# Performance work log

Measured on AMD Instinct MI355X. Metric: run time of the kernel, lower is better.

## Reference

```python
import jax, jax.numpy as jnp
import numpy as np


def bilinear_align_corners(p, H, W):
    # p: [B, C, h, w] -> [B, C, H, W], matches F.interpolate(mode='bilinear', align_corners=True)
    b, c, h, w = p.shape
    ys = jnp.linspace(0.0, h - 1.0, H)
    xs = jnp.linspace(0.0, w - 1.0, W)
    y0 = jnp.floor(ys).astype(jnp.int32)
    x0 = jnp.floor(xs).astype(jnp.int32)
    y1 = jnp.minimum(y0 + 1, h - 1)
    x1 = jnp.minimum(x0 + 1, w - 1)
    wy = (ys - y0.astype(p.dtype))[:, None]          # [H,1]
    wx = (xs - x0.astype(p.dtype))                   # [W]
    rows = p[:, :, y0, :] * (1 - wy) + p[:, :, y1, :] * wy   # [B,C,H,w]
    out = rows[:, :, :, x0] * (1 - wx) + rows[:, :, :, x1] * wx  # [B,C,H,W]
    return out


def conv1x1(x, W, b):
    return jnp.einsum('bchw,oc->bohw', x, W) + b[None, :, None, None]


def scan_axis(feat, A_bar, B_bar, axis):
    # selective recurrence h_i = A_i * stop_grad(h_{i-1}) + B_i * x_i along `axis`
    f = jnp.moveaxis(feat, axis, 0)
    A = jnp.moveaxis(A_bar, axis, 0)
    B = jnp.moveaxis(B_bar, axis, 0)

    def step(prev, inp):
        a_i, b_i, x_i = inp
        h = a_i * jax.lax.stop_gradient(prev) + b_i * x_i
        return h, h

    _, hs = jax.lax.scan(step, jnp.zeros_like(f[0]), (A, B, f))
    return jnp.moveaxis(hs, 0, axis)


def setup_inputs() -> dict:
    key = jax.random.key(0)
    ks = jax.random.split(key, 12)
    Bsz, Cin, H, W = 4, 64, 256, 256
    hid = 128
    s_in = 1.0 / np.sqrt(Cin)
    s_hid = 1.0 / np.sqrt(hid)
    return {
        'x': jax.random.normal(ks[0], (Bsz, Cin, H, W), jnp.float32),
        'prior': jax.random.normal(ks[1], (Bsz, 1, 64, 64), jnp.float32),
        'W_in': jax.random.uniform(ks[2], (hid, Cin), jnp.float32, -s_in, s_in),
        'b_in': jax.random.uniform(ks[3], (hid,), jnp.float32, -s_in, s_in),
        'W_out': jax.random.uniform(ks[4], (Cin, hid), jnp.float32, -s_hid, s_hid),
        'b_out': jax.random.uniform(ks[5], (Cin,), jnp.float32, -s_hid, s_hid),
        'W_delta': jax.random.uniform(ks[6], (hid, hid), jnp.float32, -s_hid, s_hid),
        'b_delta': jax.random.uniform(ks[7], (hid,), jnp.float32, -s_hid, s_hid),
        'W_B': jax.random.uniform(ks[8], (hid, hid), jnp.float32, -s_hid, s_hid),
        'b_B': jax.random.uniform(ks[9], (hid,), jnp.float32, -s_hid, s_hid),
        'A_param': jax.random.normal(ks[10], (hid,), jnp.float32),
        'lambda_delta': jnp.float32(0.1),
        'alpha': jnp.float32(0.1),
        'gamma': jnp.float32(0.1),
    }


def reference(x, prior, W_in, b_in, W_out, b_out, W_delta, b_delta, W_B, b_B,
              A_param, lambda_delta, alpha, gamma):
    Bsz, C, H, W = x.shape
    prior_up = jnp.clip(bilinear_align_corners(prior, H, W), -1.0, 1.0)
    x_proj = conv1x1(x, W_in, b_in)
    delta = jax.nn.softplus(conv1x1(x_proj, W_delta, b_delta) + lambda_delta * prior_up)
    B_k = conv1x1(x_proj, W_B, b_B) * (1.0 + alpha * prior_up)
    A = -jnp.exp(A_param)[None, :, None, None]
    A_bar = jnp.exp(delta * A)
    B_bar = delta * B_k
    # dim=0 in torch code scans along W (axis 3); dim=1 scans along H (axis 2)
    scanned = scan_axis(x_proj, A_bar, B_bar, 3) + scan_axis(x_proj, A_bar, B_bar, 2)
    out = conv1x1(scanned, W_out, b_out)
    return (x + gamma * out, prior_up)
```

## Files before the change

kernel.cpp:

```cpp
#include <hip/hip_runtime.h>
#include <hip/hip_bf16.h>

#define OUT1 16777216
#define BIG  33554432

typedef _Float16 half8 __attribute__((ext_vector_type(8)));
typedef float    floatx4 __attribute__((ext_vector_type(4)));

struct __align__(8) h4s { _Float16 x, y, z, w; };
struct __align__(16) au16 { h4s a, u; };

__global__ __launch_bounds__(256) void k_comb(const float* __restrict__ W_in, const float* __restrict__ b_in,
        const float* __restrict__ W_delta, const float* __restrict__ b_delta,
        const float* __restrict__ W_B, const float* __restrict__ b_B,
        const float* __restrict__ A_param, const float* __restrict__ W_out,
        _Float16* __restrict__ Wch, float* __restrict__ bcv, float* __restrict__ negA,
        _Float16* __restrict__ Wof, float* __restrict__ bct){
    int i = blockIdx.x*256 + threadIdx.x;
    if (i < 24576){
        int r = i >> 6, c = i & 63;
        float v;
        if (r < 128) v = W_in[i];
        else if (r < 256){
            int rr = r-128; float s = 0.f;
            for (int k=0;k<128;k++) s = fmaf(W_delta[(rr<<7)+k], W_in[(k<<6)+c], s);
            v = s;
        } else {
            int rr = r-256; float s = 0.f;
            for (int k=0;k<128;k++) s = fmaf(W_B[(rr<<7)+k], W_in[(k<<6)+c], s);
            v = s;
        }
        Wch[i] = (_Float16)v;
    } else if (i < 24960){
        int r = i - 24576; float v;
        if (r < 128) v = b_in[r];
        else if (r < 256){
            int rr=r-128; float s = b_delta[rr];
            for (int k=0;k<128;k++) s = fmaf(W_delta[(rr<<7)+k], b_in[k], s);
            v = s;
        } else {
            int rr=r-256; float s = b_B[rr];
            for (int k=0;k<128;k++) s = fmaf(W_B[(rr<<7)+k], b_in[k], s);
            v = s;
        }
        bcv[r] = v;
    } else if (i < 25088){
        negA[i-24960] = -expf(A_param[i-24960]);
    } else if (i < 33280){
        Wof[i-25088] = (_Float16)W_out[i-25088];
    } else if (i < 33792){
        int j = i - 33280;
        int c = j >> 2, comp = j & 3;
        float v;
        if (comp == 0) v = b_in[c];
        else if (comp == 1){
            float s = b_delta[c];
            for (int k=0;k<128;k++) s = fmaf(W_delta[(c<<7)+k], b_in[k], s);
            v = s;
        } else if (comp == 2){
            float s = b_B[c];
            for (int k=0;k<128;k++) s = fmaf(W_B[(c<<7)+k], b_in[k], s);
            v = s;
        } else {
            v = -expf(A_param[c]);
        }
        bct[j] = v;
    }
}

__global__ __launch_bounds__(512, 4) void k_proj_mfma(const float* __restrict__ x, const float* __restrict__ prior,
        const _Float16* __restrict__ Wch, const float* __restrict__ bct,
        const float* __restrict__ lam_p, const float* __restrict__ alp_p,
        float* __restrict__ pu, au16* __restrict__ AU){
    __shared__ _Float16 Ws[24576];

    const int t    = threadIdx.x;
    const int lane = t & 63;
    const int wave = t >> 6;
    const int col  = lane & 15;
    const int quad = lane >> 4;

    const int bl      = blockIdx.x;
    const int b       = bl >> 7;
    const int px_base = (bl & 127) << 9;

    {
        const float4* wsrc = (const float4*)Wch;
        #pragma unroll
        for (int i = 0; i < 6; i++){
            int c = t + (i << 9);
            int row = c >> 3, part = c & 7;
            float4 v = wsrc[c];
            int byteoff = ((row << 7) + (part << 4)) ^ ((row & 7) << 4);
            *(float4*)((char*)Ws + byteoff) = v;
        }
    }

    const float lamv = lam_p[0], alpv = alp_p[0];
    const float* xcol = x + ((size_t)b<<22) + col;

    float xf0[8], xf1[8];
    {
        const float* xp = xcol + px_base + (wave<<4);
        #pragma unroll
        for (int j = 0; j < 8; j++){
            xf0[j] = xp[(size_t)(quad*8 + j) << 16];
            xf1[j] = xp[(size_t)(quad*8 + j + 32) << 16];
        }
    }

    __syncthreads();

    const int qb = quad << 4;
    const char* wsb = (const char*)Ws;

    #pragma unroll 1
    for (int ch = 0; ch < 4; ch++){
        const int pxw = px_base + (ch << 7) + (wave << 4);

        half8 aX0, aX1;
        #pragma unroll
        for (int j = 0; j < 8; j++){
            aX0[j] = (_Float16)xf0[j];
            aX1[j] = (_Float16)xf1[j];
        }

        if (ch < 3){
            const float* xn = xcol + pxw + 128;
            #pragma unroll
            for (int j = 0; j < 8; j++){
                xf0[j] = xn[(size_t)(quad*8 + j) << 16];
                xf1[j] = xn[(size_t)(quad*8 + j + 32) << 16];
            }
        }

        const float scale = 63.0f/255.0f;
        int yy = pxw >> 8;
        float sy = yy*scale;
        int y0 = min((int)floorf(sy), 63);
        int y1 = min(y0+1, 63);
        float wy = sy - (float)y0;
        const float* pb0 = prior + (b<<12) + (y0<<6);
        const float* pb1 = prior + (b<<12) + (y1<<6);
        int xx0 = (pxw & 255) + (quad<<2);
        float lpu[4], apu[4];
        float4 puo;
        #pragma unroll
        for (int r = 0; r < 4; r++){
            float sx = (float)(xx0 + r)*scale;
            int x0 = min((int)floorf(sx), 63);
            int x1 = min(x0+1, 63);
            float wx = sx - (float)x0;
            float r0 = pb0[x0]*(1.f-wy) + pb1[x0]*wy;
            float r1 = pb0[x1]*(1.f-wy) + pb1[x1]*wy;
            float pv = fminf(fmaxf(r0*(1.f-wx) + r1*wx, -1.f), 1.f);
            ((float*)&puo)[r] = pv;
            lpu[r] = lamv * pv;
            apu[r] = fmaf(alpv, pv, 1.f);
        }
        *(float4*)(pu + (b<<16) + pxw + (quad<<2)) = puo;

        #pragma unroll 2
        for (int ct = 0; ct < 8; ct++){
            int rI = (ct << 4) + col;
            int xr = (rI & 7) << 4;
            half8 wI0 = *(const half8*)(wsb + ((( rI       << 7) +      qb) ^ xr));
            half8 wI1 = *(const half8*)(wsb + ((( rI       << 7) + 64 + qb) ^ xr));
            half8 wD0 = *(const half8*)(wsb + ((((rI + 128)<< 7) +      qb) ^ xr));
            half8 wD1 = *(const half8*)(wsb + ((((rI + 128)<< 7) + 64 + qb) ^ xr));
            half8 wB0 = *(const half8*)(wsb + ((((rI + 256)<< 7) +      qb) ^ xr));
            half8 wB1 = *(const half8*)(wsb + ((((rI + 256)<< 7) + 64 + qb) ^ xr));

            floatx4 aI = (floatx4){0.f,0.f,0.f,0.f};
            floatx4 aD = (floatx4){0.f,0.f,0.f,0.f};
            floatx4 aB = (floatx4){0.f,0.f,0.f,0.f};
            aI = __builtin_amdgcn_mfma_f32_16x16x32_f16(aX0, wI0, aI, 0, 0, 0);
            aD = __builtin_amdgcn_mfma_f32_16x16x32_f16(aX0, wD0, aD, 0, 0, 0);
            aB = __builtin_amdgcn_mfma_f32_16x16x32_f16(aX0, wB0, aB, 0, 0, 0);
            aI = __builtin_amdgcn_mfma_f32_16x16x32_f16(aX1, wI1, aI, 0, 0, 0);
            aD = __builtin_amdgcn_mfma_f32_16x16x32_f16(aX1, wD1, aD, 0, 0, 0);
            aB = __builtin_amdgcn_mfma_f32_16x16x32_f16(aX1, wB1, aB, 0, 0, 0);

            int c = (ct<<4) + col;
            float4 bv = *(const float4*)(bct + (c<<2));
            au16 ov;
            #pragma unroll
            for (int r = 0; r < 4; r++){
                float sI = aI[r] + bv.x;
                float sD = aD[r] + bv.y;
                float sB = aB[r] + bv.z;
                float dpre  = sD + lpu[r];
                float delta = fmaxf(dpre, 0.f) + __logf(1.f + __expf(-fabsf(dpre)));
                float ab    = __expf(bv.w * delta);
                float uu    = delta * sB * apu[r] * sI;
                (&ov.a.x)[r] = (_Float16)ab;
                (&ov.u.x)[r] = (_Float16)uu;
            }
            size_t u = (((size_t)((b<<7) + c)) << 14) + (pxw >> 2) + quad;
            AU[u] = ov;
        }
    }
}

__global__ __launch_bounds__(1024) void k_scan_wh(const au16* __restrict__ AU, _Float16* __restrict__ Sh){
    __shared__ _Float16 As2[16][256], Us2[16][256];
    __shared__ float    Wsc[16][256];
    __shared__ _Float16 Shs[16][256];

    const int t    = threadIdx.x;
    const int lane = t & 63;
    const int wave = t >> 6;
    const size_t plane = (size_t)blockIdx.x;
    const size_t bI = plane >> 7, cI = plane & 127;

    float Hcol = 0.f;

    const size_t ub = (plane << 14) + lane;

    au16 cur = AU[ub + ((size_t)wave << 6)];

    #pragma unroll 1
    for (int g = 0; g < 16; g++){
        au16 nxt = cur;
        if (g < 15) nxt = AU[ub + ((size_t)(((g + 1) << 4) + wave) << 6)];

        {
            float ax=(float)cur.a.x, ay=(float)cur.a.y, az=(float)cur.a.z, aw=(float)cur.a.w;
            float ux=(float)cur.u.x, uy=(float)cur.u.y, uz=(float)cur.u.z, uw=(float)cur.u.w;

            float A = ax, U = ux;
            U = fmaf(ay, U, uy); A *= ay;
            U = fmaf(az, U, uz); A *= az;
            U = fmaf(aw, U, uw); A *= aw;
            #pragma unroll
            for (int off=1; off<64; off<<=1){
                float Apv = __shfl_up(A, off, 64);
                float Upv = __shfl_up(U, off, 64);
                if (lane >= off){ U = fmaf(A, Upv, U); A *= Apv; }
            }
            float h = __shfl_up(U, 1, 64);
            if (lane == 0) h = 0.f;
            float4 o;
            h = fmaf(ax, h, ux); o.x = h;
            h = fmaf(ay, h, uy); o.y = h;
            h = fmaf(az, h, uz); o.z = h;
            h = fmaf(aw, h, uw); o.w = h;

            int c0 = lane << 2;
            *(h4s*)&As2[wave][c0] = cur.a;
            *(h4s*)&Us2[wave][c0] = cur.u;
            *(float4*)&Wsc[wave][c0] = o;
        }

        asm volatile("s_waitcnt lgkmcnt(0)" ::: "memory");
        __builtin_amdgcn_sched_barrier(0);
        __builtin_amdgcn_s_barrier();
        __builtin_amdgcn_sched_barrier(0);

        if (t < 256){
            #pragma unroll
            for (int v = 0; v < 16; v++){
                Hcol = fmaf((float)As2[v][t], Hcol, (float)Us2[v][t]);
                Shs[v][t] = (_Float16)(Hcol + Wsc[v][t]);
            }
        }

        asm volatile("s_waitcnt lgkmcnt(0)" ::: "memory");
        __builtin_amdgcn_sched_barrier(0);
        __builtin_amdgcn_s_barrier();
        __builtin_amdgcn_sched_barrier(0);

        {
            h4s sv = *(h4s*)&Shs[wave][lane << 2];
            size_t hh = (size_t)((g << 4) + wave);
            *(h4s*)(Sh + (bI<<23) + (hh<<15) + (cI<<8) + (lane<<2)) = sv;
        }

        cur = nxt;
    }
}

__global__ __launch_bounds__(256, 4) void k_out_mfma(const float* __restrict__ x, const _Float16* __restrict__ Sh,
        const _Float16* __restrict__ Wof, const float* __restrict__ bout, const float* __restrict__ gam_p,
        float* __restrict__ out){
    const int t    = threadIdx.x;
    const int lane = t & 63;
    const int wave = t >> 6;
    const int col  = lane & 15;
    const int quad = lane >> 4;
    const int b    = blockIdx.x >> 8;
    const int hh   = blockIdx.x & 255;
    const int p0   = hh << 8;
    const int wn0  = wave << 6;

    const _Float16* shb = Sh + ((size_t)b<<23) + ((size_t)hh<<15);

    floatx4 acc[4][4];
    #pragma unroll
    for (int mt = 0; mt < 4; mt++)
        #pragma unroll
        for (int nt = 0; nt < 4; nt++)
            acc[mt][nt] = (floatx4){0.f,0.f,0.f,0.f};

    #pragma unroll
    for (int kc = 0; kc < 4; kc++){
        half8 af[4];
        #pragma unroll
        for (int mt = 0; mt < 4; mt++)
            #pragma unroll
            for (int j = 0; j < 8; j++)
                af[mt][j] = shb[((kc*32 + quad*8 + j)<<8) + wn0 + mt*16 + col];
        half8 bf[4];
        #pragma unroll
        for (int nt = 0; nt < 4; nt++)
            bf[nt] = *(const half8*)(Wof + (nt*16 + col)*128 + kc*32 + quad*8);
        #pragma unroll
        for (int mt = 0; mt < 4; mt++)
            #pragma unroll
            for (int nt = 0; nt < 4; nt++)
                acc[mt][nt] = __builtin_amdgcn_mfma_f32_16x16x32_f16(af[mt], bf[nt], acc[mt][nt], 0, 0, 0);
    }

    const float gv = gam_p[0];
    #pragma unroll
    for (int nt = 0; nt < 4; nt++){
        int o = nt*16 + col;
        float bo = bout[o];
        #pragma unroll
        for (int mt = 0; mt < 4; mt++){
            size_t idx = (((size_t)(b*64 + o))<<16) + p0 + wn0 + mt*16 + (quad<<2);
            float4 xv = *(const float4*)(x + idx);
            float4 ov;
            ov.x = fmaf(gv, acc[mt][nt][0] + bo, xv.x);
            ov.y = fmaf(gv, acc[mt][nt][1] + bo, xv.y);
            ov.z = fmaf(gv, acc[mt][nt][2] + bo, xv.z);
            ov.w = fmaf(gv, acc[mt][nt][3] + bo, xv.w);
            *(float4*)(out + idx) = ov;
        }
    }
}

extern "C" void kernel_launch(void* const* d_in, const int* in_sizes, int n_in,
                              void* d_out, int out_size, void* d_ws, size_t ws_size,
                              hipStream_t stream){
    const float* x       = (const float*)d_in[0];
    const float* prior   = (const float*)d_in[1];
    const float* W_in    = (const float*)d_in[2];
    const float* b_in    = (const float*)d_in[3];
    const float* W_out   = (const float*)d_in[4];
    const float* b_out   = (const float*)d_in[5];
    const float* W_delta = (const float*)d_in[6];
    const float* b_delta = (const float*)d_in[7];
    const float* W_B     = (const float*)d_in[8];
    const float* b_B     = (const float*)d_in[9];
    const float* A_param = (const float*)d_in[10];
    const float* lam     = (const float*)d_in[11];
    const float* alp     = (const float*)d_in[12];
    const float* gam     = (const float*)d_in[13];

    float* out = (float*)d_out;
    float* pu  = out + OUT1;

    float* ws        = (float*)d_ws;
    _Float16* Wch    = (_Float16*)ws;
    float* bcv       = ws + 12288;
    float* negA      = ws + 12672;
    _Float16* Wof    = (_Float16*)(ws + 12800);
    float* bct       = ws + 16896;
    au16* AU         = (au16*)(ws + 32768);
    _Float16* Sh     = (_Float16*)(AU + BIG/4);

    hipLaunchKernelGGL(k_comb,   dim3(132),   dim3(256), 0, stream, W_in, b_in, W_delta, b_delta,
                       W_B, b_B, A_param, W_out, Wch, bcv, negA, Wof, bct);
    hipLaunchKernelGGL(k_proj_mfma, dim3(512), dim3(512), 0, stream,
                       x, prior, Wch, bct, lam, alp, pu, AU);
    hipLaunchKernelGGL(k_scan_wh, dim3(512), dim3(1024), 0, stream, AU, Sh);
    hipLaunchKernelGGL(k_out_mfma, dim3(1024), dim3(256), 0, stream, x, Sh, Wof, b_out, gam, out);
}
```

Baseline: 270.3 us.

## Fuse projection, scan and output kernels into one cooperative persistent kernel

Merges the projection, 2D scan and output projection kernels into one cooperative kernel of 256 blocks × 1024 threads. Grid-wide syncs separate the phases, and the phases share one LDS union. Each block now handles two of the old projection blocks, two scan planes and four output tiles, which removes two kernel launches and their gaps. It also drops the unused bias and negA precompute from the weight-combine kernel. The costs are lower occupancy than the separate launches, grid.sync overhead, and a 1024-thread block for the MFMA phases, which may raise register pressure under the launch bound.

Result: slower. 620.6 us (+129.6%).

```diff
diff --git a/kernel.cpp b/kernel.cpp
--- a/kernel.cpp
+++ b/kernel.cpp
@@ -1,8 +1,11 @@
 #include <hip/hip_runtime.h>
 #include <hip/hip_bf16.h>
+#include <hip/hip_cooperative_groups.h>
 
 #define OUT1 16777216
 #define BIG  33554432
+
+namespace cg = cooperative_groups;
 
 typedef _Float16 half8 __attribute__((ext_vector_type(8)));
 typedef float    floatx4 __attribute__((ext_vector_type(4)));
@@ -14,8 +17,7 @@
         const float* __restrict__ W_delta, const float* __restrict__ b_delta,
         const float* __restrict__ W_B, const float* __restrict__ b_B,
         const float* __restrict__ A_param, const float* __restrict__ W_out,
-        _Float16* __restrict__ Wch, float* __restrict__ bcv, float* __restrict__ negA,
-        _Float16* __restrict__ Wof, float* __restrict__ bct){
+        _Float16* __restrict__ Wch, _Float16* __restrict__ Wof, float* __restrict__ bct){
     int i = blockIdx.x*256 + threadIdx.x;
     if (i < 24576){
         int r = i >> 6, c = i & 63;
@@ -31,25 +33,10 @@
             v = s;
         }
         Wch[i] = (_Float16)v;
-    } else if (i < 24960){
-        int r = i - 24576; float v;
-        if (r < 128) v = b_in[r];
-        else if (r < 256){
-            int rr=r-128; float s = b_delta[rr];
-            for (int k=0;k<128;k++) s = fmaf(W_delta[(rr<<7)+k], b_in[k], s);
-            v = s;
-        } else {
-            int rr=r-256; float s = b_B[rr];
-            for (int k=0;k<128;k++) s = fmaf(W_B[(rr<<7)+k], b_in[k], s);
-            v = s;
-        }
-        bcv[r] = v;
-    } else if (i < 25088){
-        negA[i-24960] = -expf(A_param[i-24960]);
+    } else if (i < 32768){
+        Wof[i-24576] = (_Float16)W_out[i-24576];
     } else if (i < 33280){
-        Wof[i-25088] = (_Float16)W_out[i-25088];
-    } else if (i < 33792){
-        int j = i - 33280;
+        int j = i - 32768;
         int c = j >> 2, comp = j & 3;
         float v;
         if (comp == 0) v = b_in[c];
@@ -68,274 +55,280 @@
     }
 }
 
-__global__ __launch_bounds__(512, 4) void k_proj_mfma(const float* __restrict__ x, const float* __restrict__ prior,
+union MegaLds {
+    _Float16 Ws[24576];
+    struct {
+        _Float16 As2[16][256], Us2[16][256];
+        float    Wsc[16][256];
+        _Float16 Shs[16][256];
+    } s;
+};
+
+__global__ __launch_bounds__(1024, 4) void k_mega(const float* __restrict__ x, const float* __restrict__ prior,
         const _Float16* __restrict__ Wch, const float* __restrict__ bct,
         const float* __restrict__ lam_p, const float* __restrict__ alp_p,
-        float* __restrict__ pu, au16* __restrict__ AU){
-    __shared__ _Float16 Ws[24576];
+        float* __restrict__ pu, au16* __restrict__ AU, _Float16* __restrict__ Sh,
+        const _Float16* __restrict__ Wof, const float* __restrict__ bout,
+        const float* __restrict__ gam_p, float* __restrict__ out){
+    __shared__ MegaLds L;
+    cg::grid_group grid = cg::this_grid();
 
     const int t    = threadIdx.x;
     const int lane = t & 63;
-    const int wave = t >> 6;
+    const int w16  = t >> 6;
     const int col  = lane & 15;
     const int quad = lane >> 4;
-
-    const int bl      = blockIdx.x;
-    const int b       = bl >> 7;
-    const int px_base = (bl & 127) << 9;
 
     {
         const float4* wsrc = (const float4*)Wch;
         #pragma unroll
-        for (int i = 0; i < 6; i++){
-            int c = t + (i << 9);
+        for (int i = 0; i < 3; i++){
+            int c = t + (i << 10);
             int row = c >> 3, part = c & 7;
             float4 v = wsrc[c];
             int byteoff = ((row << 7) + (part << 4)) ^ ((row & 7) << 4);
-            *(float4*)((char*)Ws + byteoff) = v;
+            *(float4*)((char*)L.Ws + byteoff) = v;
+        }
+
+        const float lamv = lam_p[0], alpv = alp_p[0];
+        const int qb = quad << 4;
+        const char* wsb = (const char*)L.Ws;
+        bool staged_sync = false;
+
+        #pragma unroll 1
+        for (int sp = 0; sp < 2; sp++){
+            const int bl      = blockIdx.x*2 + sp;
+            const int b       = bl >> 7;
+            const int px_base = (bl & 127) << 9;
+            const float* xcol = x + ((size_t)b<<22) + col;
+
+            float xf0[8], xf1[8];
+            {
+                const float* xp = xcol + px_base + (w16<<4);
+                #pragma unroll
+                for (int j = 0; j < 8; j++){
+                    xf0[j] = xp[(size_t)(quad*8 + j) << 16];
+                    xf1[j] = xp[(size_t)(quad*8 + j + 32) << 16];
+                }
+            }
+            if (!staged_sync){ __syncthreads(); staged_sync = true; }
+
+            #pragma unroll 1
+            for (int ch = 0; ch < 2; ch++){
+                const int pxw = px_base + (ch << 8) + (w16 << 4);
+
+                half8 aX0, aX1;
+                #pragma unroll
+                for (int j = 0; j < 8; j++){
+                    aX0[j] = (_Float16)xf0[j];
+                    aX1[j] = (_Float16)xf1[j];
+                }
+                if (ch < 1){
+                    const float* xn = xcol + pxw + 256;
+                    #pragma unroll
+                    for (int j = 0; j < 8; j++){
+                        xf0[j] = xn[(size_t)(quad*8 + j) << 16];
+                        xf1[j] = xn[(size_t)(quad*8 + j + 32) << 16];
+                    }
+                }
+
+                const float scale = 63.0f/255.0f;
+                int yy = pxw >> 8;
+                float sy = yy*scale;
+                int y0 = min((int)floorf(sy), 63);
+                int y1 = min(y0+1, 63);
+                float wy = sy - (float)y0;
+                const float* pb0 = prior + (b<<12) + (y0<<6);
+                const float* pb1 = prior + (b<<12) + (y1<<6);
+                int xx0 = (pxw & 255) + (quad<<2);
+                float lpu[4], apu[4];
+                float4 puo;
+                #pragma unroll
+                for (int r = 0; r < 4; r++){
+                    float sx = (float)(xx0 + r)*scale;
+                    int x0 = min((int)floorf(sx), 63);
+                    int x1 = min(x0+1, 63);
+                    float wx = sx - (float)x0;
+                    float r0 = pb0[x0]*(1.f-wy) + pb1[x0]*wy;
+                    float r1 = pb0[x1]*(1.f-wy) + pb1[x1]*wy;
+                    float pv = fminf(fmaxf(r0*(1.f-wx) + r1*wx, -1.f), 1.f);
+                    ((float*)&puo)[r] = pv;
+                    lpu[r] = lamv * pv;
+                    apu[r] = fmaf(alpv, pv, 1.f);
+                }
+                *(float4*)(pu + (b<<16) + pxw + (quad<<2)) = puo;
+
+                #pragma unroll 2
+                for (int ct = 0; ct < 8; ct++){
+                    int rI = (ct << 4) + col;
+                    int xr = (rI & 7) << 4;
+                    half8 wI0 = *(const half8*)(wsb + ((( rI       << 7) +      qb) ^ xr));
+                    half8 wI1 = *(const half8*)(wsb + ((( rI       << 7) + 64 + qb) ^ xr));
+                    half8 wD0 = *(const half8*)(wsb + ((((rI + 128)<< 7) +      qb) ^ xr));
+                    half8 wD1 = *(const half8*)(wsb + ((((rI + 128)<< 7) + 64 + qb) ^ xr));
+                    half8 wB0 = *(const half8*)(wsb + ((((rI + 256)<< 7) +      qb) ^ xr));
+                    half8 wB1 = *(const half8*)(wsb + ((((rI + 256)<< 7) + 64 + qb) ^ xr));
+
+                    floatx4 aI = (floatx4){0.f,0.f,0.f,0.f};
+                    floatx4 aD = (floatx4){0.f,0.f,0.f,0.f};
+                    floatx4 aB = (floatx4){0.f,0.f,0.f,0.f};
+                    aI = __builtin_amdgcn_mfma_f32_16x16x32_f16(aX0, wI0, aI, 0, 0, 0);
+                    aD = __builtin_amdgcn_mfma_f32_16x16x32_f16(aX0, wD0, aD, 0, 0, 0);
+                    aB = __builtin_amdgcn_mfma_f32_16x16x32_f16(aX0, wB0, aB, 0, 0, 0);
+                    aI = __builtin_amdgcn_mfma_f32_16x16x32_f16(aX1, wI1, aI, 0, 0, 0);
+                    aD = __builtin_amdgcn_mfma_f32_16x16x32_f16(aX1, wD1, aD, 0, 0, 0);
+                    aB = __builtin_amdgcn_mfma_f32_16x16x32_f16(aX1, wB1, aB, 0, 0, 0);
+
+                    int c = (ct<<4) + col;
+                    float4 bv = *(const float4*)(bct + (c<<2));
+                    au16 ov;
+                    #pragma unroll
+                    for (int r = 0; r < 4; r++){
+                        float sI = aI[r] + bv.x;
+                        float sD = aD[r] + bv.y;
+                        float sB = aB[r] + bv.z;
+                        float dpre  = sD + lpu[r];
+                        float delta = fmaxf(dpre, 0.f) + __logf(1.f + __expf(-fabsf(dpre)));
+                        float ab    = __expf(bv.w * delta);
+                        float uu    = delta * sB * apu[r] * sI;
+                        (&ov.a.x)[r] = (_Float16)ab;
+                        (&ov.u.x)[r] = (_Float16)uu;
+                    }
+                    size_t u = (((size_t)((b<<7) + c)) << 14) + (pxw >> 2) + quad;
+                    AU[u] = ov;
+                }
+            }
         }
     }
 
-    const float lamv = lam_p[0], alpv = alp_p[0];
-    const float* xcol = x + ((size_t)b<<22) + col;
-
-    float xf0[8], xf1[8];
+    __threadfence();
+    grid.sync();
+
+    #pragma unroll 1
+    for (int pp = 0; pp < 2; pp++){
+        const size_t plane = (size_t)(blockIdx.x*2 + pp);
+        const size_t bI = plane >> 7, cI = plane & 127;
+        float Hcol = 0.f;
+        const size_t ub = (plane << 14) + lane;
+
+        au16 cur = AU[ub + ((size_t)w16 << 6)];
+
+        #pragma unroll 1
+        for (int g = 0; g < 16; g++){
+            au16 nxt = cur;
+            if (g < 15) nxt = AU[ub + ((size_t)(((g + 1) << 4) + w16) << 6)];
+
+            {
+                float ax=(float)cur.a.x, ay=(float)cur.a.y, az=(float)cur.a.z, aw=(float)cur.a.w;
+                float ux=(float)cur.u.x, uy=(float)cur.u.y, uz=(float)cur.u.z, uw=(float)cur.u.w;
+
+                float A = ax, U = ux;
+                U = fmaf(ay, U, uy); A *= ay;
+                U = fmaf(az, U, uz); A *= az;
+                U = fmaf(aw, U, uw); A *= aw;
+                #pragma unroll
+                for (int off=1; off<64; off<<=1){
+                    float Apv = __shfl_up(A, off, 64);
+                    float Upv = __shfl_up(U, off, 64);
+                    if (lane >= off){ U = fmaf(A, Upv, U); A *= Apv; }
+                }
+                float h = __shfl_up(U, 1, 64);
+                if (lane == 0) h = 0.f;
+                float4 o;
+                h = fmaf(ax, h, ux); o.x = h;
+                h = fmaf(ay, h, uy); o.y = h;
+                h = fmaf(az, h, uz); o.z = h;
+                h = fmaf(aw, h, uw); o.w = h;
+
+                int c0 = lane << 2;
+                *(h4s*)&L.s.As2[w16][c0] = cur.a;
+                *(h4s*)&L.s.Us2[w16][c0] = cur.u;
+                *(float4*)&L.s.Wsc[w16][c0] = o;
+            }
+
+            asm volatile("s_waitcnt lgkmcnt(0)" ::: "memory");
+            __builtin_amdgcn_sched_barrier(0);
+            __builtin_amdgcn_s_barrier();
+            __builtin_amdgcn_sched_barrier(0);
+
+            if (t < 256){
+                #pragma unroll
+                for (int v = 0; v < 16; v++){
+                    Hcol = fmaf((float)L.s.As2[v][t], Hcol, (float)L.s.Us2[v][t]);
+                    L.s.Shs[v][t] = (_Float16)(Hcol + L.s.Wsc[v][t]);
+                }
+            }
+
+            asm volatile("s_waitcnt lgkmcnt(0)" ::: "memory");
+            __builtin_amdgcn_sched_barrier(0);
+            __builtin_amdgcn_s_barrier();
+            __builtin_amdgcn_sched_barrier(0);
+
+            {
+                h4s sv = *(h4s*)&L.s.Shs[w16][lane << 2];
+                size_t hh = (size_t)((g << 4) + w16);
+                *(h4s*)(Sh + (bI<<23) + (hh<<15) + (cI<<8) + (lane<<2)) = sv;
+            }
+
+            cur = nxt;
+        }
+    }
+
+    __threadfence();
+    grid.sync();
+
     {
-        const float* xp = xcol + px_base + (wave<<4);
-        #pragma unroll
-        for (int j = 0; j < 8; j++){
-            xf0[j] = xp[(size_t)(quad*8 + j) << 16];
-            xf1[j] = xp[(size_t)(quad*8 + j + 32) << 16];
-        }
-    }
-
-    __syncthreads();
-
-    const int qb = quad << 4;
-    const char* wsb = (const char*)Ws;
-
-    #pragma unroll 1
-    for (int ch = 0; ch < 4; ch++){
-        const int pxw = px_base + (ch << 7) + (wave << 4);
-
-        half8 aX0, aX1;
-        #pragma unroll
-        for (int j = 0; j < 8; j++){
-            aX0[j] = (_Float16)xf0[j];
-            aX1[j] = (_Float16)xf1[j];
-        }
-
-        if (ch < 3){
-            const float* xn = xcol + pxw + 128;
-            #pragma unroll
-            for (int j = 0; j < 8; j++){
-                xf0[j] = xn[(size_t)(quad*8 + j) << 16];
-                xf1[j] = xn[(size_t)(quad*8 + j + 32) << 16];
-            }
-        }
-
-        const float scale = 63.0f/255.0f;
-        int yy = pxw >> 8;
-        float sy = yy*scale;
-        int y0 = min((int)floorf(sy), 63);
-        int y1 = min(y0+1, 63);
-        float wy = sy - (float)y0;
-        const float* pb0 = prior + (b<<12) + (y0<<6);
-        const float* pb1 = prior + (b<<12) + (y1<<6);
-        int xx0 = (pxw & 255) + (quad<<2);
-        float lpu[4], apu[4];
-        float4 puo;
-        #pragma unroll
-        for (int r = 0; r < 4; r++){
-            float sx = (float)(xx0 + r)*scale;
-            int x0 = min((int)floorf(sx), 63);
-            int x1 = min(x0+1, 63);
-            float wx = sx - (float)x0;
-            float r0 = pb0[x0]*(1.f-wy) + pb1[x0]*wy;
-            float r1 = pb0[x1]*(1.f-wy) + pb1[x1]*wy;
-            float pv = fminf(fmaxf(r0*(1.f-wx) + r1*wx, -1.f), 1.f);
-            ((float*)&puo)[r] = pv;
-            lpu[r] = lamv * pv;
-            apu[r] = fmaf(alpv, pv, 1.f);
-        }
-        *(float4*)(pu + (b<<16) + pxw + (quad<<2)) = puo;
-
-        #pragma unroll 2
-        for (int ct = 0; ct < 8; ct++){
-            int rI = (ct << 4) + col;
-            int xr = (rI & 7) << 4;
-            half8 wI0 = *(const half8*)(wsb + ((( rI       << 7) +      qb) ^ xr));
-            half8 wI1 = *(const half8*)(wsb + ((( rI       << 7) + 64 + qb) ^ xr));
-            half8 wD0 = *(const half8*)(wsb + ((((rI + 128)<< 7) +      qb) ^ xr));
-            half8 wD1 = *(const half8*)(wsb + ((((rI + 128)<< 7) + 64 + qb) ^ xr));
-            half8 wB0 = *(const half8*)(wsb + ((((rI + 256)<< 7) +      qb) ^ xr));
-            half8 wB1 = *(const half8*)(wsb + ((((rI + 256)<< 7) + 64 + qb) ^ xr));
-
-            floatx4 aI = (floatx4){0.f,0.f,0.f,0.f};
-            floatx4 aD = (floatx4){0.f,0.f,0.f,0.f};
-            floatx4 aB = (floatx4){0.f,0.f,0.f,0.f};
-            aI = __builtin_amdgcn_mfma_f32_16x16x32_f16(aX0, wI0, aI, 0, 0, 0);
-            aD = __builtin_amdgcn_mfma_f32_16x16x32_f16(aX0, wD0, aD, 0, 0, 0);
-            aB = __builtin_amdgcn_mfma_f32_16x16x32_f16(aX0, wB0, aB, 0, 0, 0);
-            aI = __builtin_amdgcn_mfma_f32_16x16x32_f16(aX1, wI1, aI, 0, 0, 0);
-            aD = __builtin_amdgcn_mfma_f32_16x16x32_f16(aX1, wD1, aD, 0, 0, 0);
-            aB = __builtin_amdgcn_mfma_f32_16x16x32_f16(aX1, wB1, aB, 0, 0, 0);
-
-            int c = (ct<<4) + col;
-            float4 bv = *(const float4*)(bct + (c<<2));
-            au16 ov;
-            #pragma unroll
-            for (int r = 0; r < 4; r++){
-                float sI = aI[r] + bv.x;
-                float sD = aD[r] + bv.y;
-                float sB = aB[r] + bv.z;
-                float dpre  = sD + lpu[r];
-                float delta = fmaxf(dpre, 0.f) + __logf(1.f + __expf(-fabsf(dpre)));
-                float ab    = __expf(bv.w * delta);
-                float uu    = delta * sB * apu[r] * sI;
-                (&ov.a.x)[r] = (_Float16)ab;
-                (&ov.u.x)[r] = (_Float16)uu;
-            }
-            size_t u = (((size_t)((b<<7) + c)) << 14) + (pxw >> 2) + quad;
-            AU[u] = ov;
-        }
-    }
-}
-
-__global__ __launch_bounds__(1024) void k_scan_wh(const au16* __restrict__ AU, _Float16* __restrict__ Sh){
-    __shared__ _Float16 As2[16][256], Us2[16][256];
-    __shared__ float    Wsc[16][256];
-    __shared__ _Float16 Shs[16][256];
-
-    const int t    = threadIdx.x;
-    const int lane = t & 63;
-    const int wave = t >> 6;
-    const size_t plane = (size_t)blockIdx.x;
-    const size_t bI = plane >> 7, cI = plane & 127;
-
-    float Hcol = 0.f;
-
-    const size_t ub = (plane << 14) + lane;
-
-    au16 cur = AU[ub + ((size_t)wave << 6)];
-
-    #pragma unroll 1
-    for (int g = 0; g < 16; g++){
-        au16 nxt = cur;
-        if (g < 15) nxt = AU[ub + ((size_t)(((g + 1) << 4) + wave) << 6)];
-
-        {
-            float ax=(float)cur.a.x, ay=(float)cur.a.y, az=(float)cur.a.z, aw=(float)cur.a.w;
-            float ux=(float)cur.u.x, uy=(float)cur.u.y, uz=(float)cur.u.z, uw=(float)cur.u.w;
-
-            float A = ax, U = ux;
-            U = fmaf(ay, U, uy); A *= ay;
-            U = fmaf(az, U, uz); A *= az;
-            U = fmaf(aw, U, uw); A *= aw;
-            #pragma unroll
-            for (int off=1; off<64; off<<=1){
-                float Apv = __shfl_up(A, off, 64);
-                float Upv = __shfl_up(U, off, 64);
-                if (lane >= off){ U = fmaf(A, Upv, U); A *= Apv; }
-            }
-            float h = __shfl_up(U, 1, 64);
-            if (lane == 0) h = 0.f;
-            float4 o;
-            h = fmaf(ax, h, ux); o.x = h;
-            h = fmaf(ay, h, uy); o.y = h;
-            h = fmaf(az, h, uz); o.z = h;
-            h = fmaf(aw, h, uw); o.w = h;
-
-            int c0 = lane << 2;
-            *(h4s*)&As2[wave][c0] = cur.a;
-            *(h4s*)&Us2[wave][c0] = cur.u;
-            *(float4*)&Wsc[wave][c0] = o;
-        }
-
-        asm volatile("s_waitcnt lgkmcnt(0)" ::: "memory");
-        __builtin_amdgcn_sched_barrier(0);
-        __builtin_amdgcn_s_barrier();
-        __builtin_amdgcn_sched_barrier(0);
-
-        if (t < 256){
-            #pragma unroll
-            for (int v = 0; v < 16; v++){
-                Hcol = fmaf((float)As2[v][t], Hcol, (float)Us2[v][t]);
-                Shs[v][t] = (_Float16)(Hcol + Wsc[v][t]);
-            }
-        }
-
-        asm volatile("s_waitcnt lgkmcnt(0)" ::: "memory");
-        __builtin_amdgcn_sched_barrier(0);
-        __builtin_amdgcn_s_barrier();
-        __builtin_amdgcn_sched_barrier(0);
-
-        {
-            h4s sv = *(h4s*)&Shs[wave][lane << 2];
-            size_t hh = (size_t)((g << 4) + wave);
-            *(h4s*)(Sh + (bI<<23) + (hh<<15) + (cI<<8) + (lane<<2)) = sv;
-        }
-
-        cur = nxt;
-    }
-}
-
-__global__ __launch_bounds__(256, 4) void k_out_mfma(const float* __restrict__ x, const _Float16* __restrict__ Sh,
-        const _Float16* __restrict__ Wof, const float* __restrict__ bout, const float* __restrict__ gam_p,
-        float* __restrict__ out){
-    const int t    = threadIdx.x;
-    const int lane = t & 63;
-    const int wave = t >> 6;
-    const int col  = lane & 15;
-    const int quad = lane >> 4;
-    const int b    = blockIdx.x >> 8;
-    const int hh   = blockIdx.x & 255;
-    const int p0   = hh << 8;
-    const int wn0  = wave << 6;
-
-    const _Float16* shb = Sh + ((size_t)b<<23) + ((size_t)hh<<15);
-
-    floatx4 acc[4][4];
-    #pragma unroll
-    for (int mt = 0; mt < 4; mt++)
-        #pragma unroll
-        for (int nt = 0; nt < 4; nt++)
-            acc[mt][nt] = (floatx4){0.f,0.f,0.f,0.f};
-
-    #pragma unroll
-    for (int kc = 0; kc < 4; kc++){
-        half8 af[4];
+        const int old_idx = blockIdx.x*4 + (t >> 8);
+        const int b    = old_idx >> 8;
+        const int hh   = old_idx & 255;
+        const int p0   = hh << 8;
+        const int w4   = (t >> 6) & 3;
+        const int wn0  = w4 << 6;
+
+        const _Float16* shb = Sh + ((size_t)b<<23) + ((size_t)hh<<15);
+
+        floatx4 acc[4][4];
         #pragma unroll
         for (int mt = 0; mt < 4; mt++)
             #pragma unroll
-            for (int j = 0; j < 8; j++)
-                af[mt][j] = shb[((kc*32 + quad*8 + j)<<8) + wn0 + mt*16 + col];
-        half8 bf[4];
+            for (int nt = 0; nt < 4; nt++)
+                acc[mt][nt] = (floatx4){0.f,0.f,0.f,0.f};
+
         #pragma unroll
-        for (int nt = 0; nt < 4; nt++)
-            bf[nt] = *(const half8*)(Wof + (nt*16 + col)*128 + kc*32 + quad*8);
+        for (int kc = 0; kc < 4; kc++){
+            half8 af[4];
+            #pragma unroll
+            for (int mt = 0; mt < 4; mt++)
+                #pragma unroll
+                for (int j = 0; j < 8; j++)
+                    af[mt][j] = shb[((kc*32 + quad*8 + j)<<8) + wn0 + mt*16 + col];
+            half8 bf[4];
+            #pragma unroll
+            for (int nt = 0; nt < 4; nt++)
+                bf[nt] = *(const half8*)(Wof + (nt*16 + col)*128 + kc*32 + quad*8);
+            #pragma unroll
+            for (int mt = 0; mt < 4; mt++)
+                #pragma unroll
+                for (int nt = 0; nt < 4; nt++)
+                    acc[mt][nt] = __builtin_amdgcn_mfma_f32_16x16x32_f16(af[mt], bf[nt], acc[mt][nt], 0, 0, 0);
+        }
+
+        const float gv = gam_p[0];
         #pragma unroll
-        for (int mt = 0; mt < 4; mt++)
-            #pragma unroll
-            for (int nt = 0; nt < 4; nt++)
-                acc[mt][nt] = __builtin_amdgcn_mfma_f32_16x16x32_f16(af[mt], bf[nt], acc[mt][nt], 0, 0, 0);
-    }
-
-    const float gv = gam_p[0];
-    #pragma unroll
-    for (int nt = 0; nt < 4; nt++){
-        int o = nt*16 + col;
-        float bo = bout[o];
-        #pragma unroll
-        for (int mt = 0; mt < 4; mt++){
-            size_t idx = (((size_t)(b*64 + o))<<16) + p0 + wn0 + mt*16 + (quad<<2);
-            float4 xv = *(const float4*)(x + idx);
-            float4 ov;
-            ov.x = fmaf(gv, acc[mt][nt][0] + bo, xv.x);
-            ov.y = fmaf(gv, acc[mt][nt][1] + bo, xv.y);
-            ov.z = fmaf(gv, acc[mt][nt][2] + bo, xv.z);
-            ov.w = fmaf(gv, acc[mt][nt][3] + bo, xv.w);
-            *(float4*)(out + idx) = ov;
+        for (int nt = 0; nt < 4; nt++){
+            int o = nt*16 + col;
+            float bo = bout[o];
+            #pragma unroll
+            for (int mt = 0; mt < 4; mt++){
+                size_t idx = (((size_t)(b*64 + o))<<16) + p0 + wn0 + mt*16 + (quad<<2);
+                float4 xv = *(const float4*)(x + idx);
+                float4 ov;
+                ov.x = fmaf(gv, acc[mt][nt][0] + bo, xv.x);
+                ov.y = fmaf(gv, acc[mt][nt][1] + bo, xv.y);
+                ov.z = fmaf(gv, acc[mt][nt][2] + bo, xv.z);
+                ov.w = fmaf(gv, acc[mt][nt][3] + bo, xv.w);
+                *(float4*)(out + idx) = ov;
+            }
         }
     }
 }
@@ -363,17 +356,16 @@
 
     float* ws        = (float*)d_ws;
     _Float16* Wch    = (_Float16*)ws;
-    float* bcv       = ws + 12288;
-    float* negA      = ws + 12672;
     _Float16* Wof    = (_Float16*)(ws + 12800);
     float* bct       = ws + 16896;
     au16* AU         = (au16*)(ws + 32768);
     _Float16* Sh     = (_Float16*)(AU + BIG/4);
 
-    hipLaunchKernelGGL(k_comb,   dim3(132),   dim3(256), 0, stream, W_in, b_in, W_delta, b_delta,
-                       W_B, b_B, A_param, W_out, Wch, bcv, negA, Wof, bct);
-    hipLaunchKernelGGL(k_proj_mfma, dim3(512), dim3(512), 0, stream,
-                       x, prior, Wch, bct, lam, alp, pu, AU);
-    hipLaunchKernelGGL(k_scan_wh, dim3(512), dim3(1024), 0, stream, AU, Sh);
-    hipLaunchKernelGGL(k_out_mfma, dim3(1024), dim3(256), 0, stream, x, Sh, Wof, b_out, gam, out);
+    hipLaunchKernelGGL(k_comb, dim3(130), dim3(256), 0, stream, W_in, b_in, W_delta, b_delta,
+                       W_B, b_B, A_param, W_out, Wch, Wof, bct);
+
+    void* args[] = { (void*)&x, (void*)&prior, (void*)&Wch, (void*)&bct, (void*)&lam, (void*)&alp,
+                     (void*)&pu, (void*)&AU, (void*)&Sh, (void*)&Wof, (void*)&b_out,
+                     (void*)&gam, (void*)&out };
+    hipLaunchCooperativeKernel((void*)k_mega, dim3(256), dim3(1024), args, 0, stream);
 }
```
